# Kernel optimization log

Hardware: AMD Instinct MI355X
Metric: run time of the kernel (lower is better)

Reference implementation:

```python
import jax, jax.numpy as jnp
import numpy as np

BN_EPS = 1e-5

def _bn_relu(x, gamma, beta):
    # x: [E, B, F]; BatchNorm1d in training mode: batch stats over B, biased var
    mu = jnp.mean(x, axis=1, keepdims=True)
    var = jnp.mean(jnp.square(x - mu), axis=1, keepdims=True)
    y = gamma[:, None, :] * (x - mu) * jax.lax.rsqrt(var + BN_EPS) + beta[:, None, :]
    return jax.nn.relu(y)

def setup_inputs() -> dict:
    key = jax.random.key(0)
    ks = jax.random.split(key, 4)
    B, D, E, H1, H2, T = 32768, 1472, 8, 512, 256, 2
    s1 = (2.0 / D) ** 0.5
    s2 = (2.0 / H1) ** 0.5
    return {
        "x_deep": jax.random.normal(ks[0], (B, D), jnp.float32),
        "W1": jax.random.normal(ks[1], (E, D, H1), jnp.float32) * s1,
        "b1": jnp.zeros((E, H1), jnp.float32),
        "g1": jnp.ones((E, H1), jnp.float32),
        "be1": jnp.zeros((E, H1), jnp.float32),
        "W2": jax.random.normal(ks[2], (E, H1, H2), jnp.float32) * s2,
        "b2": jnp.zeros((E, H2), jnp.float32),
        "g2": jnp.ones((E, H2), jnp.float32),
        "be2": jnp.zeros((E, H2), jnp.float32),
        "Wg": jax.random.normal(ks[3], (T, D, E), jnp.float32) * s1,
        "bg": jnp.zeros((T, E), jnp.float32),
    }

def reference(x_deep, W1, b1, g1, be1, W2, b2, g2, be2, Wg, bg):
    # Experts: batched over expert dim E (replaces Python loop over nn.ModuleList)
    h = jnp.einsum('bd,edh->ebh', x_deep, W1) + b1[:, None, :]   # [E,B,H1]
    h = _bn_relu(h, g1, be1)                                     # dropout: identity (eval)
    h = jnp.einsum('ebh,ehk->ebk', h, W2) + b2[:, None, :]       # [E,B,H2]
    experts_out = _bn_relu(h, g2, be2)                           # [E,B,H2]
    # Gates: [T,B,E], softmax over experts
    gates = jax.nn.softmax(jnp.einsum('bd,tde->tbe', x_deep, Wg) + bg[:, None, :], axis=-1)
    # Combine: task_out[t] = reshape(experts_out * gate[...,None], [B, E*H2])
    task = experts_out[None, :, :, :] * jnp.transpose(gates, (0, 2, 1))[:, :, :, None]  # [T,E,B,H2]
    T, E, B, H2 = task.shape
    out = jnp.transpose(task, (0, 2, 1, 3)).reshape(T, B, E * H2)  # [T,B,E*H2]
    return out
```

## Files before the change

kernel.cpp:

```cpp
#include <hip/hip_runtime.h>
#include <cstdint>


typedef __attribute__((ext_vector_type(8))) __bf16 bf16x8;
typedef __attribute__((ext_vector_type(4))) float f32x4;

__device__ __forceinline__ unsigned short f2bf(float f) {
  unsigned int u = __float_as_uint(f);
  u += 0x7fffu + ((u >> 16) & 1u);
  return (unsigned short)(u >> 16);
}

__device__ __forceinline__ void async16(const void* g, void* l) {
  __builtin_amdgcn_global_load_lds((__attribute__((address_space(1))) unsigned int*)g,
                                   (__attribute__((address_space(3))) unsigned int*)l,
                                   16, 0, 0);
}

__global__ void convert_f32_bf16(const float* __restrict__ in,
                                 unsigned short* __restrict__ out, size_t n) {
  size_t i = ((size_t)blockIdx.x * blockDim.x + threadIdx.x) * 4;
  if (i + 3 < n) {
    float4 v = *(const float4*)(in + i);
    unsigned int w0 = (unsigned int)f2bf(v.x) | ((unsigned int)f2bf(v.y) << 16);
    unsigned int w1 = (unsigned int)f2bf(v.z) | ((unsigned int)f2bf(v.w) << 16);
    *(uint2*)(out + i) = make_uint2(w0, w1);
  }
}

__global__ void transpose_bf16(const float* __restrict__ W,
                               unsigned short* __restrict__ Wt, int D, int H) {
  __shared__ float tile[32][33];
  int e = blockIdx.z;
  int d0 = blockIdx.x * 32, h0 = blockIdx.y * 32;
  const float* We = W + (size_t)e * D * H;
  unsigned short* Wte = Wt + (size_t)e * D * H;
  int tx = threadIdx.x, ty = threadIdx.y;
#pragma unroll
  for (int i = 0; i < 4; ++i)
    tile[ty + i * 8][tx] = We[(size_t)(d0 + ty + i * 8) * H + h0 + tx];
  __syncthreads();
#pragma unroll
  for (int i = 0; i < 4; ++i)
    Wte[(size_t)(h0 + ty + i * 8) * D + d0 + tx] = f2bf(tile[tx][ty + i * 8]);
}

__global__ void transpose_wg(const float* __restrict__ Wg,
                             unsigned short* __restrict__ Wt, int D) {
  int idx = blockIdx.x * 256 + threadIdx.x;
  int te = idx / D, d = idx - te * D;
  int t = te >> 3, e = te & 7;
  Wt[(size_t)te * D + d] = f2bf(Wg[((size_t)t * D + d) * 8 + e]);
}

__global__ __launch_bounds__(512, 2) void gemm256(
    const unsigned short* __restrict__ A, int lda,
    const unsigned short* __restrict__ Bt,
    unsigned short* __restrict__ C, int ldc, int K,
    size_t aStrideE, size_t bStrideE, size_t cStrideE,
    float* __restrict__ sum, float* __restrict__ sq,
    int statStrideE, int statCols, int groupM, int GN) {
  __shared__ __attribute__((aligned(128))) char smem[131072];
  const int tid = threadIdx.x;
  const int lane = tid & 63;
  const int wid = tid >> 6;
  const int wm = wid & 1;
  const int wn = wid >> 1;
  const int e = blockIdx.z;

  int bx, by;
  if (groupM) {
    int bid = blockIdx.x;
    int cpx = (int)gridDim.x >> 3;
    int b2 = (bid & 7) * cpx + (bid >> 3);
    int gsize = groupM * GN;
    int gid = b2 / gsize;
    int rem = b2 - gid * gsize;
    bx = gid * groupM + rem % groupM;
    by = rem / groupM;
  } else {
    bx = blockIdx.x; by = blockIdx.y;
  }

  const unsigned short* Ae = A + (size_t)e * aStrideE + (size_t)bx * 256 * lda;
  const unsigned short* Be = Bt + (size_t)e * bStrideE + (size_t)by * 256 * K;

  const int srow = tid >> 2;
  const int scol = ((tid & 3) ^ ((tid >> 3) & 3)) * 8;
  const unsigned short* gA0 = Ae + (size_t)srow * lda + scol;
  const unsigned short* gA1 = Ae + (size_t)(srow + 128) * lda + scol;
  const unsigned short* gB0 = Be + (size_t)srow * K + scol;
  const unsigned short* gB1 = Be + (size_t)(srow + 128) * K + scol;
  char* ldsStage = smem + tid * 16;

  const int mrow = lane & 15;
  const int cb = (((lane >> 4) ^ ((lane >> 1) & 3)) << 4);
  const char* rdA = smem + (wm * 128 + mrow) * 64 + cb;
  const char* rdB = smem + 16384 + (wn * 64 + mrow) * 64 + cb;

  f32x4 acc[8][4] = {};
  const int NT = K >> 5;

  auto stage = [&](int tt) {
    char* dst = ldsStage + (tt & 3) * 32768;
    const int ko = tt * 32;
    async16(gA0 + ko, dst);
    async16(gA1 + ko, dst + 8192);
    async16(gB0 + ko, dst + 16384);
    async16(gB1 + ko, dst + 24576);
  };
  auto compute = [&](int t) {
    const char* pa = rdA + (t & 3) * 32768;
    const char* pb = rdB + (t & 3) * 32768;
    bf16x8 af[8], bfr[4];
#pragma unroll
    for (int i = 0; i < 8; ++i) af[i] = *(const bf16x8*)(pa + i * 1024);
#pragma unroll
    for (int j = 0; j < 4; ++j) bfr[j] = *(const bf16x8*)(pb + j * 1024);
    __builtin_amdgcn_s_setprio(1);
#pragma unroll
    for (int i = 0; i < 8; ++i)
#pragma unroll
      for (int j = 0; j < 4; ++j)
        acc[i][j] = __builtin_amdgcn_mfma_f32_16x16x32_bf16(af[i], bfr[j], acc[i][j], 0, 0, 0);
    __builtin_amdgcn_s_setprio(0);
  };

  stage(0); stage(1);
  asm volatile("s_waitcnt vmcnt(4)\n\ts_barrier" ::: "memory");

  int t = 0;
  for (; t < NT - 2; ++t) {
    stage(t + 2);
    compute(t);
    asm volatile("s_waitcnt vmcnt(4)\n\ts_barrier" ::: "memory");
  }
  compute(t);
  asm volatile("s_waitcnt vmcnt(0)\n\ts_barrier" ::: "memory");
  ++t;
  compute(t);

  unsigned short* Ce = C + (size_t)e * cStrideE + (size_t)bx * 256 * ldc +
                       (size_t)by * 256;
  const int r0 = wm * 128 + (lane >> 4) * 4;
  const int c0 = wn * 64 + mrow;
#pragma unroll
  for (int i = 0; i < 8; ++i)
#pragma unroll
    for (int j = 0; j < 4; ++j)
#pragma unroll
      for (int r = 0; r < 4; ++r)
        Ce[(size_t)(r0 + i * 16 + r) * ldc + c0 + j * 16] = f2bf(acc[i][j][r]);

  float* se = sum + (size_t)e * statStrideE;
  float* qe = sq + (size_t)e * statStrideE;
#pragma unroll
  for (int j = 0; j < 4; ++j) {
    float s = 0.f, q = 0.f;
#pragma unroll
    for (int i = 0; i < 8; ++i)
#pragma unroll
      for (int r = 0; r < 4; ++r) {
        float v = acc[i][j][r];
        s += v;
        q = fmaf(v, v, q);
      }
    s += __shfl_xor(s, 16, 64); s += __shfl_xor(s, 32, 64);
    q += __shfl_xor(q, 16, 64); q += __shfl_xor(q, 32, 64);
    if ((lane >> 4) == 0) {
      int col = by * 256 + wn * 64 + j * 16 + mrow;
      if (col < statCols) {
        atomicAdd(&se[col], s);
        atomicAdd(&qe[col], q);
      }
    }
  }
}

__global__ void bn_coef(const float* __restrict__ sum, const float* __restrict__ sq,
                        const float* __restrict__ g, const float* __restrict__ be,
                        float* __restrict__ A, float* __restrict__ C, int n, float invB) {
  int i = blockIdx.x * blockDim.x + threadIdx.x;
  if (i < n) {
    float mean = sum[i] * invB;
    float var = sq[i] * invB - mean * mean;
    float a = g[i] * rsqrtf(var + 1e-5f);
    A[i] = a;
    C[i] = be[i] - mean * a;
  }
}

__global__ __launch_bounds__(256) void gates_mfma(
    const unsigned short* __restrict__ xb,
    const unsigned short* __restrict__ wgt,
    const float* __restrict__ bg,
    float* __restrict__ gates, int Bn) {
  const int lane = threadIdx.x & 63;
  const int w = threadIdx.x >> 6;
  const int row0 = blockIdx.x * 64 + w * 16;
  const int mrow = lane & 15, kseg = (lane >> 4) * 8;
  const unsigned short* pa = xb + (size_t)(row0 + mrow) * 1472 + kseg;
  const unsigned short* pb = wgt + (size_t)mrow * 1472 + kseg;
  f32x4 acc = {};
  bf16x8 a0 = *(const bf16x8*)pa, b0 = *(const bf16x8*)pb;
  for (int ks = 1; ks < 46; ++ks) {
    bf16x8 a1 = *(const bf16x8*)(pa + ks * 32);
    bf16x8 b1 = *(const bf16x8*)(pb + ks * 32);
    acc = __builtin_amdgcn_mfma_f32_16x16x32_bf16(a0, b0, acc, 0, 0, 0);
    a0 = a1; b0 = b1;
  }
  acc = __builtin_amdgcn_mfma_f32_16x16x32_bf16(a0, b0, acc, 0, 0, 0);
  const int c = lane & 15;
  const float bias = bg[c];
#pragma unroll
  for (int r = 0; r < 4; ++r) {
    float v = acc[r] + bias;
    float m = v;
    m = fmaxf(m, __shfl_xor(m, 1, 64));
    m = fmaxf(m, __shfl_xor(m, 2, 64));
    m = fmaxf(m, __shfl_xor(m, 4, 64));
    float p = expf(v - m);
    float s = p;
    s += __shfl_xor(s, 1, 64);
    s += __shfl_xor(s, 2, 64);
    s += __shfl_xor(s, 4, 64);
    int rowg = row0 + (lane >> 4) * 4 + r;
    gates[((size_t)(c >> 3) * Bn + rowg) * 8 + (c & 7)] = p / s;
  }
}

__global__ void bn_relu_inplace(unsigned short* __restrict__ h, const float* __restrict__ A,
                                const float* __restrict__ C) {
  int tid = blockIdx.x * blockDim.x + threadIdx.x;
  int r = tid >> 9, cb = tid & 511;
  int col = cb * 8;
  size_t i = (size_t)r * 4096 + col;
  uint4 v = *(const uint4*)(h + i);
  unsigned int w[4] = {v.x, v.y, v.z, v.w};
#pragma unroll
  for (int j = 0; j < 4; ++j) {
    float f0 = __uint_as_float(w[j] << 16);
    float f1 = __uint_as_float(w[j] & 0xffff0000u);
    float y0 = fmaxf(fmaf(A[col + 2 * j], f0, C[col + 2 * j]), 0.f);
    float y1 = fmaxf(fmaf(A[col + 2 * j + 1], f1, C[col + 2 * j + 1]), 0.f);
    w[j] = (unsigned int)f2bf(y0) | ((unsigned int)f2bf(y1) << 16);
  }
  *(uint4*)(h + i) = make_uint4(w[0], w[1], w[2], w[3]);
}

__global__ void combine(const unsigned short* __restrict__ h2,
                        const float* __restrict__ A, const float* __restrict__ C,
                        const float* __restrict__ gates,
                        float* __restrict__ out, int Bn) {
  int b = blockIdx.x;
  int c = threadIdx.x * 8;
  int e = c >> 8;
  uint4 v = *(const uint4*)(h2 + (size_t)b * 2048 + c);
  unsigned int w[4] = {v.x, v.y, v.z, v.w};
  float y[8];
#pragma unroll
  for (int j = 0; j < 4; ++j) {
    float f0 = __uint_as_float(w[j] << 16);
    float f1 = __uint_as_float(w[j] & 0xffff0000u);
    y[2 * j]     = fmaxf(fmaf(A[c + 2 * j], f0, C[c + 2 * j]), 0.f);
    y[2 * j + 1] = fmaxf(fmaf(A[c + 2 * j + 1], f1, C[c + 2 * j + 1]), 0.f);
  }
  float g0 = gates[(size_t)b * 8 + e];
  float g1 = gates[((size_t)Bn + b) * 8 + e];
  float4* o0 = (float4*)(out + (size_t)b * 2048 + c);
  float4* o1 = (float4*)(out + ((size_t)Bn + b) * 2048 + c);
  o0[0] = make_float4(y[0] * g0, y[1] * g0, y[2] * g0, y[3] * g0);
  o0[1] = make_float4(y[4] * g0, y[5] * g0, y[6] * g0, y[7] * g0);
  o1[0] = make_float4(y[0] * g1, y[1] * g1, y[2] * g1, y[3] * g1);
  o1[1] = make_float4(y[4] * g1, y[5] * g1, y[6] * g1, y[7] * g1);
}

extern "C" void kernel_launch(void* const* d_in, const int* in_sizes, int n_in,
                              void* d_out, int out_size, void* d_ws, size_t ws_size,
                              hipStream_t stream) {
  const int B = 32768, D = 1472, E = 8, H1 = 512, H2 = 256;
  const int N1 = E * H1;
  const float* x   = (const float*)d_in[0];
  const float* W1  = (const float*)d_in[1];
  const float* g1  = (const float*)d_in[3];
  const float* be1 = (const float*)d_in[4];
  const float* W2  = (const float*)d_in[5];
  const float* g2  = (const float*)d_in[7];
  const float* be2 = (const float*)d_in[8];
  const float* Wg  = (const float*)d_in[9];
  const float* bg  = (const float*)d_in[10];
  float* out = (float*)d_out;

  char* p = (char*)d_ws;
  unsigned short* x_b = (unsigned short*)p; p += (size_t)B * D * 2;
  unsigned short* W1t = (unsigned short*)p; p += (size_t)N1 * D * 2;
  unsigned short* Wgt = (unsigned short*)p; p += (size_t)16 * D * 2;
  unsigned short* W2t = (unsigned short*)p; p += (size_t)E * H2 * H1 * 2;
  unsigned short* h1b = (unsigned short*)p; p += (size_t)B * N1 * 2;
  unsigned short* h2b = (unsigned short*)p; p += (size_t)B * E * H2 * 2;
  float* gatesBuf = (float*)p; p += (size_t)2 * B * 8 * 4;
  float* sum1 = (float*)p; p += (size_t)N1 * 4;
  float* sq1  = (float*)p; p += (size_t)N1 * 4;
  float* sum2 = (float*)p; p += (size_t)E * H2 * 4;
  float* sq2  = (float*)p; p += (size_t)E * H2 * 4;
  float* A1   = (float*)p; p += (size_t)N1 * 4;
  float* C1   = (float*)p; p += (size_t)N1 * 4;
  float* A2   = (float*)p; p += (size_t)E * H2 * 4;
  float* C2   = (float*)p; p += (size_t)E * H2 * 4;

  hipMemsetAsync(sum1, 0, (size_t)(2 * N1 + 2 * E * H2) * 4, stream);

  convert_f32_bf16<<<(unsigned)((size_t)B * D / 1024), 256, 0, stream>>>(
      x, x_b, (size_t)B * D);
  transpose_bf16<<<dim3(D / 32, H1 / 32, E), dim3(32, 8), 0, stream>>>(W1, W1t, D, H1);
  transpose_wg<<<16 * D / 256, 256, 0, stream>>>(Wg, Wgt, D);
  transpose_bf16<<<dim3(H1 / 32, H2 / 32, E), dim3(32, 8), 0, stream>>>(W2, W2t, H1, H2);

  gemm256<<<dim3(128 * 16), 512, 0, stream>>>(
      x_b, D, W1t, h1b, N1, D, (size_t)0, (size_t)0, (size_t)0,
      sum1, sq1, 0, N1, 16, 16);

  bn_coef<<<N1 / 256, 256, 0, stream>>>(sum1, sq1, g1, be1, A1, C1, N1, 1.f / B);
  gates_mfma<<<B / 64, 256, 0, stream>>>(x_b, Wgt, bg, gatesBuf, B);
  bn_relu_inplace<<<(unsigned)((size_t)B * 512 / 256), 256, 0, stream>>>(h1b, A1, C1);

  gemm256<<<dim3(B / 256, 1, E), 512, 0, stream>>>(
      h1b, N1, W2t, h2b, E * H2, H1,
      (size_t)H1, (size_t)H1 * H2, (size_t)H2,
      sum2, sq2, H2, H2, 0, 0);

  bn_coef<<<E * H2 / 256, 256, 0, stream>>>(sum2, sq2, g2, be2, A2, C2, E * H2, 1.f / B);

  combine<<<B, 256, 0, stream>>>(h2b, A2, C2, gatesBuf, out, B);
}
```

Baseline: 1.454 ms.

## Split GEMM k-slab into two half-phases interleaving LDS reads, async loads, MFMA

Restructures the main GEMM loop so each 32-wide k-slab is processed in two halves. Each half loads four A fragments, issues half of the next-next stage's async global-to-LDS copies (A then B), and runs sixteen MFMAs, with extra s_barriers between phases. The aim is to spread memory issue across the compute phase and lower peak fragment register use, so loads overlap better with MFMA. The cost is three extra workgroup barriers per slab, which could stall waves.

```diff
diff --git a/kernel.cpp b/kernel.cpp
--- a/kernel.cpp
+++ b/kernel.cpp
@@ -86,59 +86,76 @@
   const unsigned short* Be = Bt + (size_t)e * bStrideE + (size_t)by * 256 * K;
 
   const int srow = tid >> 2;
-  const int scol = ((tid & 3) ^ ((tid >> 3) & 3)) * 8;
-  const unsigned short* gA0 = Ae + (size_t)srow * lda + scol;
-  const unsigned short* gA1 = Ae + (size_t)(srow + 128) * lda + scol;
-  const unsigned short* gB0 = Be + (size_t)srow * K + scol;
-  const unsigned short* gB1 = Be + (size_t)(srow + 128) * K + scol;
-  char* ldsStage = smem + tid * 16;
+  const int scol = 8 * ((tid & 3) ^ ((tid >> 3) & 3));
+  const unsigned short* gA = Ae + (size_t)srow * lda + scol;
+  const unsigned short* gB = Be + (size_t)srow * K + scol;
+  const size_t aRow128 = (size_t)128 * lda;
+  const size_t bRow128 = (size_t)128 * K;
+  char* ldsDst = smem + tid * 16;
+
+  auto stageA = [&](int u) {
+    char* d = ldsDst + (u & 3) * 32768;
+    const unsigned short* g = gA + u * 32;
+    async16(g, d);
+    async16(g + aRow128, d + 8192);
+  };
+  auto stageB = [&](int u) {
+    char* d = ldsDst + (u & 3) * 32768 + 16384;
+    const unsigned short* g = gB + u * 32;
+    async16(g, d);
+    async16(g + bRow128, d + 8192);
+  };
 
   const int mrow = lane & 15;
-  const int cb = (((lane >> 4) ^ ((lane >> 1) & 3)) << 4);
-  const char* rdA = smem + (wm * 128 + mrow) * 64 + cb;
-  const char* rdB = smem + 16384 + (wn * 64 + mrow) * 64 + cb;
+  const int kgb = ((lane >> 4) << 4) ^ (((mrow >> 1) & 3) << 4);
+  const char* rdA = smem + (wm * 128 + mrow) * 64 + kgb;
+  const char* rdB = smem + 16384 + (wn * 64 + mrow) * 64 + kgb;
 
   f32x4 acc[8][4] = {};
-  const int NT = K >> 5;
-
-  auto stage = [&](int tt) {
-    char* dst = ldsStage + (tt & 3) * 32768;
-    const int ko = tt * 32;
-    async16(gA0 + ko, dst);
-    async16(gA1 + ko, dst + 8192);
-    async16(gB0 + ko, dst + 16384);
-    async16(gB1 + ko, dst + 24576);
-  };
-  auto compute = [&](int t) {
-    const char* pa = rdA + (t & 3) * 32768;
-    const char* pb = rdB + (t & 3) * 32768;
-    bf16x8 af[8], bfr[4];
-#pragma unroll
-    for (int i = 0; i < 8; ++i) af[i] = *(const bf16x8*)(pa + i * 1024);
+  const int NS = K >> 5;
+
+  auto slab = [&](int u, bool st) {
+    const char* pa = rdA + (u & 3) * 32768;
+    const char* pb = rdB + (u & 3) * 32768;
+    bf16x8 af[4], bfr[4];
+#pragma unroll
+    for (int i = 0; i < 4; ++i) af[i] = *(const bf16x8*)(pa + i * 1024);
 #pragma unroll
     for (int j = 0; j < 4; ++j) bfr[j] = *(const bf16x8*)(pb + j * 1024);
+    if (st) stageA(u + 2);
+    asm volatile("s_barrier" ::: "memory");
     __builtin_amdgcn_s_setprio(1);
 #pragma unroll
-    for (int i = 0; i < 8; ++i)
+    for (int i = 0; i < 4; ++i)
 #pragma unroll
       for (int j = 0; j < 4; ++j)
         acc[i][j] = __builtin_amdgcn_mfma_f32_16x16x32_bf16(af[i], bfr[j], acc[i][j], 0, 0, 0);
     __builtin_amdgcn_s_setprio(0);
+    asm volatile("s_barrier" ::: "memory");
+#pragma unroll
+    for (int i = 0; i < 4; ++i) af[i] = *(const bf16x8*)(pa + (i + 4) * 1024);
+    if (st) stageB(u + 2);
+    asm volatile("s_barrier" ::: "memory");
+    __builtin_amdgcn_s_setprio(1);
+#pragma unroll
+    for (int i = 0; i < 4; ++i)
+#pragma unroll
+      for (int j = 0; j < 4; ++j)
+        acc[i + 4][j] = __builtin_amdgcn_mfma_f32_16x16x32_bf16(af[i], bfr[j], acc[i + 4][j], 0, 0, 0);
+    __builtin_amdgcn_s_setprio(0);
   };
 
-  stage(0); stage(1);
+  stageA(0); stageB(0); stageA(1); stageB(1);
   asm volatile("s_waitcnt vmcnt(4)\n\ts_barrier" ::: "memory");
 
-  int t = 0;
-  for (; t < NT - 2; ++t) {
-    stage(t + 2);
-    compute(t);
+  int u = 0;
+  for (; u < NS - 2; ++u) {
+    slab(u, true);
     asm volatile("s_waitcnt vmcnt(4)\n\ts_barrier" ::: "memory");
   }
-  compute(t);
+  slab(u, false); ++u;
   asm volatile("s_waitcnt vmcnt(0)\n\ts_barrier" ::: "memory");
-  ++t;
-  compute(t);
+  slab(u, false);
 
   unsigned short* Ce = C + (size_t)e * cStrideE + (size_t)bx * 256 * ldc +
                        (size_t)by * 256;
```

Result: no change. 1.456 ms (+0.1%).
